# Kernel tuning notes

Measured on AMD Instinct MI355X. Metric: run time of the kernel, lower is better.

Reference implementation:

```python
import jax, jax.numpy as jnp
import numpy as np

B, T, D, H = 32, 2048, 512, 256  # batch, seq_len, in_size, hidden per direction (hidden_size=512)


def setup_inputs() -> dict:
    key = jax.random.key(0)
    ks = jax.random.split(key, 10)
    x = jax.random.normal(ks[0], (B, T, D), dtype=jnp.float32)
    # ragged lengths: zero out the padded tail so input.any(-1) recovers length
    lengths = jax.random.randint(ks[1], (B,), T // 2, T + 1)
    mask = jnp.arange(T)[None, :] < lengths[:, None]
    x = x * mask[..., None]
    s = 1.0 / np.sqrt(H)
    u = lambda k, shape: jax.random.uniform(k, shape, jnp.float32, -s, s)
    return {
        "x": x,
        "Wf_ih": u(ks[2], (4 * H, D)), "Wf_hh": u(ks[3], (4 * H, H)),
        "bf_ih": u(ks[4], (4 * H,)),   "bf_hh": u(ks[5], (4 * H,)),
        "Wb_ih": u(ks[6], (4 * H, D)), "Wb_hh": u(ks[7], (4 * H, H)),
        "bb_ih": u(ks[8], (4 * H,)),   "bb_hh": u(ks[9], (4 * H,)),
    }


def _run_lstm(xs, Wih, Whh, bih, bhh):
    # xs: [B, T, D] -> outputs [B, T, H]; vectorized over batch inside scan
    b = xs.shape[0]
    h0 = jnp.zeros((b, H), xs.dtype)
    c0 = jnp.zeros((b, H), xs.dtype)

    def step(carry, x_t):
        h, c = carry
        z = x_t @ Wih.T + h @ Whh.T + bih + bhh  # [B, 4H]
        i, f, g, o = jnp.split(z, 4, axis=-1)
        c = jax.nn.sigmoid(f) * c + jax.nn.sigmoid(i) * jnp.tanh(g)
        h = jax.nn.sigmoid(o) * jnp.tanh(c)
        return (h, c), h

    _, ys = jax.lax.scan(step, (h0, c0), jnp.swapaxes(xs, 0, 1))  # [T, B, H]
    return jnp.swapaxes(ys, 0, 1)


def _flip_padded(seq, length):
    # flip first `length` timesteps, keep zero padding at the tail
    return jnp.roll(jnp.flip(seq, axis=0), length, axis=0)


def reference(x, Wf_ih, Wf_hh, bf_ih, bf_hh, Wb_ih, Wb_hh, bb_ih, bb_hh):
    lengths = jnp.sum(jnp.any(x != 0, axis=-1), axis=-1)  # [B]
    fwd = _run_lstm(x, Wf_ih, Wf_hh, bf_ih, bf_hh)
    xr = jax.vmap(_flip_padded)(x, lengths)
    bwd = _run_lstm(xr, Wb_ih, Wb_hh, bb_ih, bb_hh)
    return jnp.concatenate([fwd, bwd], axis=-1)  # [B, T, 2H]
```

## Files before the change

### kernel.cpp

```cpp
#include <hip/hip_runtime.h>
#include <hip/hip_fp16.h>


typedef _Float16 f16;
typedef _Float16 f16x2 __attribute__((ext_vector_type(2)));
typedef _Float16 f16x4 __attribute__((ext_vector_type(4)));
typedef _Float16 f16x8 __attribute__((ext_vector_type(8)));
typedef float    f32x4 __attribute__((ext_vector_type(4)));

#define NB   32
#define NT   2048
#define ND   512
#define NH   256
#define NG   1024
#define MTOT 65536

#define OFF_PRE   0UL
#define SZ_PRE    (65536UL * 2048UL * 2UL)
#define OFF_WALL  (OFF_PRE + SZ_PRE)
#define SZ_WALL   (2048UL * 512UL * 2UL)
#define OFF_WP    (OFF_WALL + SZ_WALL)
#define SZ_WP     (2UL * 192UL * 512UL * 4UL)
#define OFF_WLDS  (OFF_WP + SZ_WP)
#define SZ_WLDS   (2UL * 16384UL * 8UL)
#define OFF_BSUM  (OFF_WLDS + SZ_WLDS)
#define SZ_BSUM   (2048UL * 4UL)
#define OFF_FLAGS (OFF_BSUM + SZ_BSUM)
#define SZ_FLAGS  (65536UL * 4UL)
#define OFF_LEN   (OFF_FLAGS + SZ_FLAGS)
#define SZ_LEN    (128UL)
#define OFF_Z     (OFF_LEN + SZ_LEN)
#define SZ_Z      (16UL)

#if __has_builtin(__builtin_amdgcn_fdot2)
#define FDOT2(a, b, c) __builtin_amdgcn_fdot2((a), (b), (c), false)
#else
#define FDOT2(a, b, c) ((c) + (float)(a)[0] * (float)(b)[0] + (float)(a)[1] * (float)(b)[1])
#endif

__device__ __forceinline__ float sigm_f(float x) {
    float t = __expf(-fabsf(x));
    float s = 1.0f / (1.0f + t);
    return x >= 0.0f ? s : 1.0f - s;
}
__device__ __forceinline__ float tanh_f(float x) {
    float t = __expf(-2.0f * fabsf(x));
    float r = (1.0f - t) / (1.0f + t);
    return x >= 0.0f ? r : -r;
}

__global__ void k_flags(const float* __restrict__ x, int* __restrict__ flags) {
    int bt = blockIdx.x;
    int i  = threadIdx.x;
    float2 v = ((const float2*)(x + (size_t)bt * ND))[i];
    int nz = (v.x != 0.0f) || (v.y != 0.0f);
    unsigned long long m = __ballot(nz);
    __shared__ int sf[4];
    if ((i & 63) == 0) sf[i >> 6] = (m != 0ULL);
    __syncthreads();
    if (i == 0) flags[bt] = sf[0] | sf[1] | sf[2] | sf[3];
}

__global__ void k_lenred(const int* __restrict__ flags, int* __restrict__ lengths) {
    int b = blockIdx.x, i = threadIdx.x;
    int s = 0;
#pragma unroll
    for (int k = 0; k < 8; ++k) s += flags[b * NT + i + k * 256];
    for (int o = 32; o > 0; o >>= 1) s += __shfl_down(s, o);
    __shared__ int sp[4];
    if ((i & 63) == 0) sp[i >> 6] = s;
    __syncthreads();
    if (i == 0) lengths[b] = sp[0] + sp[1] + sp[2] + sp[3];
}

__global__ void k_wall(const float* __restrict__ Wf, const float* __restrict__ Wb,
                       f16* __restrict__ wall) {
    int idx = blockIdx.x * 256 + threadIdx.x;
    int e4 = idx * 4;
    int n = e4 >> 9, k = e4 & 511;
    const float* src = (n < 1024 ? Wf + (size_t)n * 512 : Wb + (size_t)(n - 1024) * 512) + k;
    float4 v = *(const float4*)src;
    f16x4 o;
    o[0] = (f16)v.x; o[1] = (f16)v.y; o[2] = (f16)v.z; o[3] = (f16)v.w;
    *(f16x4*)(wall + (size_t)n * 512 + k) = o;
}

__global__ void k_repack(const float* __restrict__ Wfhh, const float* __restrict__ Wbhh,
                         const float* __restrict__ bfi, const float* __restrict__ bfh,
                         const float* __restrict__ bbi, const float* __restrict__ bbh,
                         f16x2* __restrict__ wp, uint2* __restrict__ wldsg,
                         float* __restrict__ bsum, unsigned int* __restrict__ zslot) {
    int blk = blockIdx.x, tid = threadIdx.x;
    if (blk < 384) {
        int dir = blk / 192, e = blk % 192;
        const float* W = dir ? Wbhh : Wfhh;
        int r = e / 96, c = e % 96;
        int row = tid + r * 512;
        f16x2 v;
        v[0] = (f16)W[row * 256 + 2 * c];
        v[1] = (f16)W[row * 256 + 2 * c + 1];
        wp[((size_t)(dir * 192 + e)) * 512 + tid] = v;
    } else if (blk < 448) {
        int idx = (blk - 384) * 512 + tid;
        int dir = idx >> 14, rem = idx & 16383;
        int top = rem >> 10, row = rem & 1023;
        int kb = 192 + (top >> 1) * 8 + (top & 1) * 4;
        const float* W = dir ? Wbhh : Wfhh;
        f16x2 lo, hi;
        lo[0] = (f16)W[row * 256 + kb + 0]; lo[1] = (f16)W[row * 256 + kb + 1];
        hi[0] = (f16)W[row * 256 + kb + 2]; hi[1] = (f16)W[row * 256 + kb + 3];
        uint2 u;
        u.x = __builtin_bit_cast(unsigned int, lo);
        u.y = __builtin_bit_cast(unsigned int, hi);
        wldsg[(size_t)dir * 16384 + rem] = u;
    } else if (blk < 452) {
        int idx = (blk - 448) * 512 + tid;
        int dir = idx >> 10, g = idx & 1023;
        bsum[idx] = dir ? (bbi[g] + bbh[g]) : (bfi[g] + bfh[g]);
    } else {
        if (tid < 4) zslot[tid] = 0u;
    }
}

__launch_bounds__(512, 2)
__global__ void k_gemm(const float* __restrict__ X, const f16* __restrict__ Wall,
                       f16* __restrict__ Pre) {
    __shared__ f16 Al[2][128 * 32];
    __shared__ f16 Bl[2][128 * 32];
    int bid = blockIdx.x;
    int mblk = bid >> 4, nblk = bid & 15;
    int m0 = mblk * 128, n0 = nblk * 128;
    int tid = threadIdx.x;
    int lane = tid & 63, w = tid >> 6;
    int wm = w >> 2, wn = w & 3;
    int sr = tid >> 2, skq = tid & 3;
    const float* xsrc = X + (size_t)(m0 + sr) * ND + skq * 8;
    const f16*  bsrc = Wall + (size_t)(n0 + (tid >> 2)) * ND + (tid & 3) * 8;

    f32x4 acc[4][2];
#pragma unroll
    for (int a = 0; a < 4; ++a)
#pragma unroll
        for (int b = 0; b < 2; ++b) acc[a][b] = (f32x4){0.f, 0.f, 0.f, 0.f};

    {
        float4 v0 = *(const float4*)(xsrc);
        float4 v1 = *(const float4*)(xsrc + 4);
        f16x8 bv = *(const f16x8*)(bsrc);
        f16x8 h8;
        h8[0] = (f16)v0.x; h8[1] = (f16)v0.y; h8[2] = (f16)v0.z; h8[3] = (f16)v0.w;
        h8[4] = (f16)v1.x; h8[5] = (f16)v1.y; h8[6] = (f16)v1.z; h8[7] = (f16)v1.w;
        *(f16x8*)&Al[0][sr * 32 + skq * 8] = h8;
        *(f16x8*)&Bl[0][tid * 8] = bv;
        __syncthreads();
    }

    for (int kk = 0; kk < 16; ++kk) {
        int buf = kk & 1;
        float4 v0, v1; f16x8 bv;
        bool more = (kk < 15);
        if (more) {
            v0 = *(const float4*)(xsrc + (kk + 1) * 32);
            v1 = *(const float4*)(xsrc + (kk + 1) * 32 + 4);
            bv = *(const f16x8*)(bsrc + (kk + 1) * 32);
        }
        f16x8 af[4], bf[2];
#pragma unroll
        for (int mt = 0; mt < 4; ++mt)
            af[mt] = *(const f16x8*)&Al[buf][(wm * 64 + mt * 16 + (lane & 15)) * 32 + (lane >> 4) * 8];
#pragma unroll
        for (int nt = 0; nt < 2; ++nt)
            bf[nt] = *(const f16x8*)&Bl[buf][(wn * 32 + nt * 16 + (lane & 15)) * 32 + (lane >> 4) * 8];
#pragma unroll
        for (int mt = 0; mt < 4; ++mt)
#pragma unroll
            for (int nt = 0; nt < 2; ++nt)
                acc[mt][nt] = __builtin_amdgcn_mfma_f32_16x16x32_f16(af[mt], bf[nt], acc[mt][nt], 0, 0, 0);
        if (more) {
            f16x8 h8;
            h8[0] = (f16)v0.x; h8[1] = (f16)v0.y; h8[2] = (f16)v0.z; h8[3] = (f16)v0.w;
            h8[4] = (f16)v1.x; h8[5] = (f16)v1.y; h8[6] = (f16)v1.z; h8[7] = (f16)v1.w;
            *(f16x8*)&Al[buf ^ 1][sr * 32 + skq * 8] = h8;
            *(f16x8*)&Bl[buf ^ 1][tid * 8] = bv;
        }
        __syncthreads();
    }

    int col = lane & 15, rg = lane >> 4;
#pragma unroll
    for (int mt = 0; mt < 4; ++mt)
#pragma unroll
        for (int nt = 0; nt < 2; ++nt)
#pragma unroll
            for (int q = 0; q < 4; ++q) {
                int m = m0 + wm * 64 + mt * 16 + rg * 4 + q;
                int n = n0 + wn * 32 + nt * 16 + col;
                Pre[(size_t)m * 2048 + n] = (f16)acc[mt][nt][q];
            }
}

__launch_bounds__(512, 2)
__global__ void k_recur(const f16* __restrict__ Pre, const f16x2* __restrict__ wp,
                        const uint2* __restrict__ wldsg, const float* __restrict__ bsum,
                        const int* __restrict__ lengths, const f16* __restrict__ zslot,
                        float* __restrict__ out) {
    extern __shared__ char smem[];
    f16*   hbuf = (f16*)(smem + 131072);
    float* aex  = (float*)(smem + 131072 + 512);

    int bid = blockIdx.x;
    int b = bid >> 1, dir = bid & 1;
    int j = threadIdx.x;
    int L = lengths[b];

    {
        const char* src = (const char*)(wldsg + (size_t)dir * 16384);
#pragma unroll
        for (int s = 0; s < 16; ++s) {
            int q = s * 512 + j;
            *(uint4*)(smem + (size_t)q * 16) = *(const uint4*)(src + (size_t)q * 16);
        }
    }
    f16x2 wreg[192];
    {
        const f16x2* wpp = wp + (size_t)(dir * 192) * 512 + j;
#pragma unroll
        for (int e = 0; e < 192; ++e) wreg[e] = wpp[(size_t)e * 512];
    }
    float bs0 = bsum[dir * 1024 + j];
    float bs1 = bsum[dir * 1024 + j + 512];
    if (j < 32) *(uint4*)(hbuf + j * 8) = (uint4){0u, 0u, 0u, 0u};
    __syncthreads();

    float cst = 0.0f;
    const size_t baseRow = (size_t)b * NT;

    f16 pn0, pn1;
    {
        int rt = dir ? (L - 1) : 0;
        const f16* q0 = Pre + (baseRow + rt) * 2048 + dir * 1024 + j;
        pn0 = q0[0]; pn1 = q0[512];
    }

    for (int t = 0; t < NT; ++t) {
        float pre0 = (float)pn0, pre1 = (float)pn1;
        {
            int tn = t + 1;
            int rt = dir ? (L - 1 - tn) : tn;
            const f16 *q0, *q1;
            if (tn < NT && rt >= 0) {
                q0 = Pre + (baseRow + rt) * 2048 + dir * 1024 + j;
                q1 = q0 + 512;
            } else {
                q0 = zslot; q1 = zslot;
            }
            pn0 = *q0; pn1 = *q1;
        }

        float a0 = bs0 + pre0, a1 = 0.0f;
        float b0 = bs1 + pre1, b1 = 0.0f;
#pragma unroll
        for (int c = 0; c < 32; ++c) {
            f16x8 hv = *(const f16x8*)(hbuf + c * 8);
            f16x2 h2q[4];
            h2q[0][0] = hv[0]; h2q[0][1] = hv[1];
            h2q[1][0] = hv[2]; h2q[1][1] = hv[3];
            h2q[2][0] = hv[4]; h2q[2][1] = hv[5];
            h2q[3][0] = hv[6]; h2q[3][1] = hv[7];
            f16x2 w0q[4], w1q[4];
            if (c < 24) {
                w0q[0] = wreg[c * 4 + 0]; w0q[1] = wreg[c * 4 + 1];
                w0q[2] = wreg[c * 4 + 2]; w0q[3] = wreg[c * 4 + 3];
                w1q[0] = wreg[96 + c * 4 + 0]; w1q[1] = wreg[96 + c * 4 + 1];
                w1q[2] = wreg[96 + c * 4 + 2]; w1q[3] = wreg[96 + c * 4 + 3];
            } else {
                int cc = c - 24;
                uint2 u00 = *(const uint2*)(smem + ((size_t)(cc * 2 + 0) * 1024 + j) * 8);
                uint2 u01 = *(const uint2*)(smem + ((size_t)(cc * 2 + 1) * 1024 + j) * 8);
                uint2 u10 = *(const uint2*)(smem + ((size_t)(cc * 2 + 0) * 1024 + j + 512) * 8);
                uint2 u11 = *(const uint2*)(smem + ((size_t)(cc * 2 + 1) * 1024 + j + 512) * 8);
                w0q[0] = __builtin_bit_cast(f16x2, u00.x); w0q[1] = __builtin_bit_cast(f16x2, u00.y);
                w0q[2] = __builtin_bit_cast(f16x2, u01.x); w0q[3] = __builtin_bit_cast(f16x2, u01.y);
                w1q[0] = __builtin_bit_cast(f16x2, u10.x); w1q[1] = __builtin_bit_cast(f16x2, u10.y);
                w1q[2] = __builtin_bit_cast(f16x2, u11.x); w1q[3] = __builtin_bit_cast(f16x2, u11.y);
            }
            a0 = FDOT2(h2q[0], w0q[0], a0);
            b0 = FDOT2(h2q[0], w1q[0], b0);
            a1 = FDOT2(h2q[1], w0q[1], a1);
            b1 = FDOT2(h2q[1], w1q[1], b1);
            a0 = FDOT2(h2q[2], w0q[2], a0);
            b0 = FDOT2(h2q[2], w1q[2], b0);
            a1 = FDOT2(h2q[3], w0q[3], a1);
            b1 = FDOT2(h2q[3], w1q[3], b1);
        }
        float z0 = a0 + a1;
        float z1 = b0 + b1;

        if (j < 256) aex[j] = sigm_f(z0) * tanh_f(z1);
        __syncthreads();
        if (j >= 256) {
            int i = j - 256;
            cst = sigm_f(z0) * cst + aex[i];
            float h = sigm_f(z1) * tanh_f(cst);
            out[(baseRow + t) * 512 + dir * 256 + i] = h;
            hbuf[i] = (f16)h;
        }
        __syncthreads();
    }
}

extern "C" void kernel_launch(void* const* d_in, const int* in_sizes, int n_in,
                              void* d_out, int out_size, void* d_ws, size_t ws_size,
                              hipStream_t stream) {
    (void)in_sizes; (void)n_in; (void)out_size; (void)ws_size;
    const float* x     = (const float*)d_in[0];
    const float* Wf_ih = (const float*)d_in[1];
    const float* Wf_hh = (const float*)d_in[2];
    const float* bf_ih = (const float*)d_in[3];
    const float* bf_hh = (const float*)d_in[4];
    const float* Wb_ih = (const float*)d_in[5];
    const float* Wb_hh = (const float*)d_in[6];
    const float* bb_ih = (const float*)d_in[7];
    const float* bb_hh = (const float*)d_in[8];
    float* out = (float*)d_out;

    char* ws = (char*)d_ws;
    f16*          Pre    = (f16*)(ws + OFF_PRE);
    f16*          Wall   = (f16*)(ws + OFF_WALL);
    f16x2*        wp     = (f16x2*)(ws + OFF_WP);
    uint2*        wldsg  = (uint2*)(ws + OFF_WLDS);
    float*        bsum   = (float*)(ws + OFF_BSUM);
    int*          flags  = (int*)(ws + OFF_FLAGS);
    int*          lens   = (int*)(ws + OFF_LEN);
    unsigned int* zslot  = (unsigned int*)(ws + OFF_Z);

    static const size_t RECUR_LDS = 131072 + 512 + 1024;
    hipFuncSetAttribute((const void*)k_recur,
                        hipFuncAttributeMaxDynamicSharedMemorySize, (int)RECUR_LDS);

    k_flags <<<MTOT, 256, 0, stream>>>(x, flags);
    k_lenred<<<NB, 256, 0, stream>>>(flags, lens);
    k_wall  <<<1024, 256, 0, stream>>>(Wf_ih, Wb_ih, Wall);
    k_repack<<<453, 512, 0, stream>>>(Wf_hh, Wb_hh, bf_ih, bf_hh, bb_ih, bb_hh,
                                      wp, wldsg, bsum, zslot);
    k_gemm  <<<(MTOT / 128) * (2048 / 128), 512, 0, stream>>>(x, Wall, Pre);
    k_recur <<<NB * 2, 512, RECUR_LDS, stream>>>(Pre, wp, wldsg, bsum, lens,
                                                 (const f16*)zslot, out);
}
```

Measured before the change: 4.894 ms.

## Pair gate rows across adjacent lanes and double-buffer h to drop one barrier

Remaps gate rows so that each unit's i/g and f/o rows sit on adjacent lanes. The i*tanh(g) term is then exchanged with a lane shuffle instead of an LDS round trip plus a __syncthreads, which leaves one barrier per timestep instead of two. The hidden-state buffer is double-buffered by step parity so the next step's writes cannot race this step's reads. The LDS weight tail is repacked into 16-byte rows for wider loads, and launch bounds drop to one block per CU.

```diff
diff --git a/kernel.cpp b/kernel.cpp
--- a/kernel.cpp
+++ b/kernel.cpp
@@ -20,9 +20,9 @@
 #define OFF_WALL  (OFF_PRE + SZ_PRE)
 #define SZ_WALL   (2048UL * 512UL * 2UL)
 #define OFF_WP    (OFF_WALL + SZ_WALL)
-#define SZ_WP     (2UL * 192UL * 512UL * 4UL)
+#define SZ_WP    (2UL * 192UL * 512UL * 4UL)
 #define OFF_WLDS  (OFF_WP + SZ_WP)
-#define SZ_WLDS   (2UL * 16384UL * 8UL)
+#define SZ_WLDS   (2UL * 8192UL * 16UL)
 #define OFF_BSUM  (OFF_WLDS + SZ_WLDS)
 #define SZ_BSUM   (2048UL * 4UL)
 #define OFF_FLAGS (OFF_BSUM + SZ_BSUM)
@@ -85,36 +85,45 @@
     *(f16x4*)(wall + (size_t)n * 512 + k) = o;
 }
 
+__device__ __forceinline__ int gate_row(int tid, int r) {
+    int u = tid >> 1, p = tid & 1;
+    return (p ? 256 + u : u) + r * 512;
+}
+
 __global__ void k_repack(const float* __restrict__ Wfhh, const float* __restrict__ Wbhh,
                          const float* __restrict__ bfi, const float* __restrict__ bfh,
                          const float* __restrict__ bbi, const float* __restrict__ bbh,
-                         f16x2* __restrict__ wp, uint2* __restrict__ wldsg,
+                         f16x2* __restrict__ wp, uint4* __restrict__ wldsg,
                          float* __restrict__ bsum, unsigned int* __restrict__ zslot) {
     int blk = blockIdx.x, tid = threadIdx.x;
     if (blk < 384) {
         int dir = blk / 192, e = blk % 192;
         const float* W = dir ? Wbhh : Wfhh;
         int r = e / 96, c = e % 96;
-        int row = tid + r * 512;
+        int row = gate_row(tid, r);
         f16x2 v;
         v[0] = (f16)W[row * 256 + 2 * c];
         v[1] = (f16)W[row * 256 + 2 * c + 1];
         wp[((size_t)(dir * 192 + e)) * 512 + tid] = v;
-    } else if (blk < 448) {
+    } else if (blk < 416) {
         int idx = (blk - 384) * 512 + tid;
-        int dir = idx >> 14, rem = idx & 16383;
-        int top = rem >> 10, row = rem & 1023;
-        int kb = 192 + (top >> 1) * 8 + (top & 1) * 4;
+        int dir = idx >> 13, rem = idx & 8191;
+        int cc = rem >> 10, row = rem & 1023;
+        int kb = 192 + cc * 8;
         const float* W = dir ? Wbhh : Wfhh;
-        f16x2 lo, hi;
-        lo[0] = (f16)W[row * 256 + kb + 0]; lo[1] = (f16)W[row * 256 + kb + 1];
-        hi[0] = (f16)W[row * 256 + kb + 2]; hi[1] = (f16)W[row * 256 + kb + 3];
-        uint2 u;
-        u.x = __builtin_bit_cast(unsigned int, lo);
-        u.y = __builtin_bit_cast(unsigned int, hi);
-        wldsg[(size_t)dir * 16384 + rem] = u;
-    } else if (blk < 452) {
-        int idx = (blk - 448) * 512 + tid;
+        f16x2 p0, p1, p2, p3;
+        p0[0] = (f16)W[row * 256 + kb + 0]; p0[1] = (f16)W[row * 256 + kb + 1];
+        p1[0] = (f16)W[row * 256 + kb + 2]; p1[1] = (f16)W[row * 256 + kb + 3];
+        p2[0] = (f16)W[row * 256 + kb + 4]; p2[1] = (f16)W[row * 256 + kb + 5];
+        p3[0] = (f16)W[row * 256 + kb + 6]; p3[1] = (f16)W[row * 256 + kb + 7];
+        uint4 u;
+        u.x = __builtin_bit_cast(unsigned int, p0);
+        u.y = __builtin_bit_cast(unsigned int, p1);
+        u.z = __builtin_bit_cast(unsigned int, p2);
+        u.w = __builtin_bit_cast(unsigned int, p3);
+        wldsg[(size_t)dir * 8192 + rem] = u;
+    } else if (blk < 420) {
+        int idx = (blk - 416) * 512 + tid;
         int dir = idx >> 10, g = idx & 1023;
         bsum[idx] = dir ? (bbi[g] + bbh[g]) : (bfi[g] + bfh[g]);
     } else {
@@ -199,26 +208,28 @@
             }
 }
 
-__launch_bounds__(512, 2)
+__launch_bounds__(512, 1)
 __global__ void k_recur(const f16* __restrict__ Pre, const f16x2* __restrict__ wp,
-                        const uint2* __restrict__ wldsg, const float* __restrict__ bsum,
+                        const uint4* __restrict__ wldsg, const float* __restrict__ bsum,
                         const int* __restrict__ lengths, const f16* __restrict__ zslot,
                         float* __restrict__ out) {
     extern __shared__ char smem[];
-    f16*   hbuf = (f16*)(smem + 131072);
-    float* aex  = (float*)(smem + 131072 + 512);
+    f16* hbuf = (f16*)(smem + 131072);
 
     int bid = blockIdx.x;
     int b = bid >> 1, dir = bid & 1;
     int j = threadIdx.x;
+    int u = j >> 1, p = j & 1;
+    int rowA = p ? 256 + u : u;
+    int rowB = rowA + 512;
     int L = lengths[b];
 
     {
-        const char* src = (const char*)(wldsg + (size_t)dir * 16384);
+        const uint4* src = wldsg + (size_t)dir * 8192;
 #pragma unroll
         for (int s = 0; s < 16; ++s) {
             int q = s * 512 + j;
-            *(uint4*)(smem + (size_t)q * 16) = *(const uint4*)(src + (size_t)q * 16);
+            *(uint4*)(smem + (size_t)q * 16) = src[q];
         }
     }
     f16x2 wreg[192];
@@ -227,19 +238,21 @@
 #pragma unroll
         for (int e = 0; e < 192; ++e) wreg[e] = wpp[(size_t)e * 512];
     }
-    float bs0 = bsum[dir * 1024 + j];
-    float bs1 = bsum[dir * 1024 + j + 512];
-    if (j < 32) *(uint4*)(hbuf + j * 8) = (uint4){0u, 0u, 0u, 0u};
+    float bs0 = bsum[dir * 1024 + rowA];
+    float bs1 = bsum[dir * 1024 + rowB];
+    if (j < 64) *(uint4*)(hbuf + j * 8) = (uint4){0u, 0u, 0u, 0u};
     __syncthreads();
 
     float cst = 0.0f;
     const size_t baseRow = (size_t)b * NT;
+    const int colA = dir * 1024 + rowA;
+    const int colB = dir * 1024 + rowB;
 
     f16 pn0, pn1;
     {
         int rt = dir ? (L - 1) : 0;
-        const f16* q0 = Pre + (baseRow + rt) * 2048 + dir * 1024 + j;
-        pn0 = q0[0]; pn1 = q0[512];
+        const f16* q0 = Pre + (baseRow + rt) * 2048;
+        pn0 = q0[colA]; pn1 = q0[colB];
     }
 
     for (int t = 0; t < NT; ++t) {
@@ -249,19 +262,20 @@
             int rt = dir ? (L - 1 - tn) : tn;
             const f16 *q0, *q1;
             if (tn < NT && rt >= 0) {
-                q0 = Pre + (baseRow + rt) * 2048 + dir * 1024 + j;
-                q1 = q0 + 512;
+                const f16* base = Pre + (baseRow + rt) * 2048;
+                q0 = base + colA; q1 = base + colB;
             } else {
                 q0 = zslot; q1 = zslot;
             }
             pn0 = *q0; pn1 = *q1;
         }
 
+        const f16* hcur = hbuf + (t & 1) * 256;
         float a0 = bs0 + pre0, a1 = 0.0f;
         float b0 = bs1 + pre1, b1 = 0.0f;
 #pragma unroll
         for (int c = 0; c < 32; ++c) {
-            f16x8 hv = *(const f16x8*)(hbuf + c * 8);
+            f16x8 hv = *(const f16x8*)(hcur + c * 8);
             f16x2 h2q[4];
             h2q[0][0] = hv[0]; h2q[0][1] = hv[1];
             h2q[1][0] = hv[2]; h2q[1][1] = hv[3];
@@ -275,14 +289,12 @@
                 w1q[2] = wreg[96 + c * 4 + 2]; w1q[3] = wreg[96 + c * 4 + 3];
             } else {
                 int cc = c - 24;
-                uint2 u00 = *(const uint2*)(smem + ((size_t)(cc * 2 + 0) * 1024 + j) * 8);
-                uint2 u01 = *(const uint2*)(smem + ((size_t)(cc * 2 + 1) * 1024 + j) * 8);
-                uint2 u10 = *(const uint2*)(smem + ((size_t)(cc * 2 + 0) * 1024 + j + 512) * 8);
-                uint2 u11 = *(const uint2*)(smem + ((size_t)(cc * 2 + 1) * 1024 + j + 512) * 8);
-                w0q[0] = __builtin_bit_cast(f16x2, u00.x); w0q[1] = __builtin_bit_cast(f16x2, u00.y);
-                w0q[2] = __builtin_bit_cast(f16x2, u01.x); w0q[3] = __builtin_bit_cast(f16x2, u01.y);
-                w1q[0] = __builtin_bit_cast(f16x2, u10.x); w1q[1] = __builtin_bit_cast(f16x2, u10.y);
-                w1q[2] = __builtin_bit_cast(f16x2, u11.x); w1q[3] = __builtin_bit_cast(f16x2, u11.y);
+                uint4 uA = *(const uint4*)(smem + ((size_t)(cc * 1024) + rowA) * 16);
+                uint4 uB = *(const uint4*)(smem + ((size_t)(cc * 1024) + rowB) * 16);
+                w0q[0] = __builtin_bit_cast(f16x2, uA.x); w0q[1] = __builtin_bit_cast(f16x2, uA.y);
+                w0q[2] = __builtin_bit_cast(f16x2, uA.z); w0q[3] = __builtin_bit_cast(f16x2, uA.w);
+                w1q[0] = __builtin_bit_cast(f16x2, uB.x); w1q[1] = __builtin_bit_cast(f16x2, uB.y);
+                w1q[2] = __builtin_bit_cast(f16x2, uB.z); w1q[3] = __builtin_bit_cast(f16x2, uB.w);
             }
             a0 = FDOT2(h2q[0], w0q[0], a0);
             b0 = FDOT2(h2q[0], w1q[0], b0);
@@ -296,14 +308,13 @@
         float z0 = a0 + a1;
         float z1 = b0 + b1;
 
-        if (j < 256) aex[j] = sigm_f(z0) * tanh_f(z1);
-        __syncthreads();
-        if (j >= 256) {
-            int i = j - 256;
-            cst = sigm_f(z0) * cst + aex[i];
+        float a = sigm_f(z0) * tanh_f(z1);
+        float ap = __shfl_xor(a, 1);
+        if (p) {
+            cst = sigm_f(z0) * cst + ap;
             float h = sigm_f(z1) * tanh_f(cst);
-            out[(baseRow + t) * 512 + dir * 256 + i] = h;
-            hbuf[i] = (f16)h;
+            out[(baseRow + t) * 512 + dir * 256 + u] = h;
+            hbuf[((t + 1) & 1) * 256 + u] = (f16)h;
         }
         __syncthreads();
     }
@@ -328,20 +339,20 @@
     f16*          Pre    = (f16*)(ws + OFF_PRE);
     f16*          Wall   = (f16*)(ws + OFF_WALL);
     f16x2*        wp     = (f16x2*)(ws + OFF_WP);
-    uint2*        wldsg  = (uint2*)(ws + OFF_WLDS);
+    uint4*        wldsg  = (uint4*)(ws + OFF_WLDS);
     float*        bsum   = (float*)(ws + OFF_BSUM);
     int*          flags  = (int*)(ws + OFF_FLAGS);
     int*          lens   = (int*)(ws + OFF_LEN);
     unsigned int* zslot  = (unsigned int*)(ws + OFF_Z);
 
-    static const size_t RECUR_LDS = 131072 + 512 + 1024;
+    static const size_t RECUR_LDS = 131072 + 1024;
     hipFuncSetAttribute((const void*)k_recur,
                         hipFuncAttributeMaxDynamicSharedMemorySize, (int)RECUR_LDS);
 
     k_flags <<<MTOT, 256, 0, stream>>>(x, flags);
     k_lenred<<<NB, 256, 0, stream>>>(flags, lens);
     k_wall  <<<1024, 256, 0, stream>>>(Wf_ih, Wb_ih, Wall);
-    k_repack<<<453, 512, 0, stream>>>(Wf_hh, Wb_hh, bf_ih, bf_hh, bb_ih, bb_hh,
+    k_repack<<<421, 512, 0, stream>>>(Wf_hh, Wb_hh, bf_ih, bf_hh, bb_ih, bb_hh,
                                       wp, wldsg, bsum, zslot);
     k_gemm  <<<(MTOT / 128) * (2048 / 128), 512, 0, stream>>>(x, Wall, Pre);
     k_recur <<<NB * 2, 512, RECUR_LDS, stream>>>(Pre, wp, wldsg, bsum, lens,
```

After: 3.938 ms. 1.24x faster.
